# Performance work log

Measured on AMD Instinct MI355X. Metric: run time of the kernel, lower is better.

The kernel has to match this reference:

```python
import jax, jax.numpy as jnp
import numpy as np

SCORE_THRESHOLD = 0.5
GRID = 512  # spatial extent per axis; batch in {0,1} so keys fit int32
SENTINEL = np.int32(2 ** 30)  # larger than any real key (< 2**28)


def _encode(coords):
    # coords: [N,4] int32 (batch, x, y, z) -> unique int32 key
    c = coords.astype(jnp.int32)
    return ((c[:, 0] * GRID + c[:, 1]) * GRID + c[:, 2]) * GRID + c[:, 3]


def _decode_np(k):
    z = k % GRID; k = k // GRID
    y = k % GRID; k = k // GRID
    x = k % GRID; b = k // GRID
    return np.stack([b, x, y, z], axis=1).astype(np.int32)


def setup_inputs() -> dict:
    rng = np.random.default_rng(0)
    Nx, Nm, Dx = 2_000_000, 2_000_000, 16
    # draw unique coordinate keys (MinkowskiEngine coords are unique per tensor)
    keys = np.unique(rng.integers(0, 2 * GRID ** 3, size=3 * Nx, dtype=np.int64)).astype(np.int32)
    rng.shuffle(keys)
    x_keys = keys[:Nx]
    m_keys = np.concatenate([x_keys[: Nm // 2], keys[Nx: Nx + Nm - Nm // 2]])
    rng.shuffle(m_keys)
    key = jax.random.key(0)
    k1, k2 = jax.random.split(key)
    return {
        "x_C": jnp.asarray(_decode_np(x_keys)),
        "x_F": jax.random.normal(k1, (Nx, Dx), dtype=jnp.float32),
        "m_C": jnp.asarray(_decode_np(m_keys)),
        "m_F": jax.random.uniform(k2, (Nm, 1), dtype=jnp.float32),
    }


def _gather_on_union(keys, feats, union_keys):
    # scatter each tensor's features onto the union coordinate set (zeros elsewhere)
    n = keys.shape[0]
    order = jnp.argsort(keys)
    ks = keys[order]
    fs = feats[order]
    pos = jnp.searchsorted(ks, union_keys)
    pc = jnp.clip(pos, 0, n - 1)
    found = (pos < n) & (ks[pc] == union_keys)
    return jnp.where(found[:, None], fs[pc], jnp.zeros((), feats.dtype))


def reference(x_C, x_F, m_C, m_F):
    Nx, Nm = x_F.shape[0], m_F.shape[0]
    xk = _encode(x_C)
    mk = _encode(m_C)
    # coordinate union (ME sparse-tensor addition); fixed size Nx+Nm, padded w/ sentinel
    uk = jnp.unique(jnp.concatenate([xk, mk]), size=Nx + Nm, fill_value=SENTINEL)
    xf = _gather_on_union(xk, x_F, uk)   # x features on union coords  [Nu, Dx]
    mf = _gather_on_union(mk, m_F, uk)   # mask scores on union coords [Nu, 1]
    # target = score above threshold AND x has any positive feature at this coord
    target = (mf[:, 0] > SCORE_THRESHOLD) & (xf > 0).any(axis=1)
    # prune expressed as fixed-shape masking (padding rows have target=False)
    return xf * target[:, None].astype(xf.dtype)
```

## Files before the change

kernel.cpp:

```cpp
#include <hip/hip_runtime.h>
#include <stdint.h>

#define KEYSPACE     (1u << 28)
#define NBUCKET      2048u
#define BUCKET_KEYS  (KEYSPACE / NBUCKET)
#define BUCKET_WORDS (BUCKET_KEYS / 16u)
#define BUCKET_CAP   4096u
#define EPB          8192
#define UMASK        0x55555555u
#define RECS_CAP     1024u

__device__ __forceinline__ uint32_t encode4(int4 c) {
    return ((((uint32_t)c.x * 512u + (uint32_t)c.y) * 512u + (uint32_t)c.z) * 512u) + (uint32_t)c.w;
}
__device__ __forceinline__ uint32_t swz(uint32_t w) { return w ^ ((w >> 5) & 31u); }

__global__ __launch_bounds__(256) void bin_zero(const int* __restrict__ xC,
                                                const int* __restrict__ mC,
                                                const float* __restrict__ mF,
                                                uint2* __restrict__ barr,
                                                uint32_t* __restrict__ bcnt,
                                                float* __restrict__ out,
                                                uint32_t out4, int Nx, int Nm) {
    __shared__ uint32_t hist[NBUCKET];
    __shared__ uint32_t base_[NBUCKET];
    int t = threadIdx.x;
    int blk = blockIdx.x;
    uint32_t nthr = gridDim.x * 256u;

    {
        uint4 z = make_uint4(0u, 0u, 0u, 0u);
        uint4* o4 = reinterpret_cast<uint4*>(out);
        for (uint32_t q = (uint32_t)blk * 256u + t; q < out4; q += nthr) o4[q] = z;
    }

    int total = Nx + Nm;
    int start = blk * EPB;
    int end = min(start + EPB, total);

    for (int q = t; q < (int)NBUCKET; q += 256) hist[q] = 0u;
    __syncthreads();

    for (int e = start + t; e < end; e += 256) {
        uint32_t k = (e < Nx) ? encode4(reinterpret_cast<const int4*>(xC)[e])
                              : encode4(reinterpret_cast<const int4*>(mC)[e - Nx]);
        atomicAdd(&hist[k >> 17], 1u);
    }
    __syncthreads();

    for (int q = t; q < (int)NBUCKET; q += 256) {
        uint32_t h = hist[q];
        base_[q] = h ? atomicAdd(&bcnt[q], h) : 0u;
        hist[q] = 0u;
    }
    __syncthreads();

    for (int e = start + t; e < end; e += 256) {
        uint32_t k; uint2 pl;
        if (e < Nx) {
            k = encode4(reinterpret_cast<const int4*>(xC)[e]);
            pl.x = (k & (BUCKET_KEYS - 1u)) | (1u << 18);
            pl.y = (uint32_t)e;
        } else {
            int j = e - Nx;
            k = encode4(reinterpret_cast<const int4*>(mC)[j]);
            pl.x = (k & (BUCKET_KEYS - 1u)) | ((mF[j] > 0.5f) ? (1u << 17) : 0u);
            pl.y = 0u;
        }
        uint32_t b = k >> 17;
        uint32_t pos = base_[b] + atomicAdd(&hist[b], 1u);
        barr[(size_t)b * BUCKET_CAP + pos] = pl;
    }
}

__global__ __launch_bounds__(256) void build_bucket(const uint2* __restrict__ barr,
                                                    const uint32_t* __restrict__ bcnt,
                                                    uint2* __restrict__ records,
                                                    uint32_t* __restrict__ rcount,
                                                    uint32_t* __restrict__ Btot) {
    __shared__ uint32_t bmp[BUCKET_WORDS];
    __shared__ uint32_t gpre[512];
    __shared__ uint32_t sdata[256];
    __shared__ uint2 recs[RECS_CAP];
    __shared__ uint32_t nrec, rbase;
    int t = threadIdx.x;
    uint32_t b = blockIdx.x;

    {
        uint4 z = make_uint4(0u, 0u, 0u, 0u);
        uint4* bz = reinterpret_cast<uint4*>(bmp);
        for (int q = t; q < (int)(BUCKET_WORDS / 4u); q += 256) bz[q] = z;
    }
    __syncthreads();

    uint32_t n = bcnt[b];
    const uint2* ba = barr + (size_t)b * BUCKET_CAP;

    for (uint32_t e = t; e < n; e += 256u) {
        uint32_t pl = ba[e].x;
        uint32_t off = pl & (BUCKET_KEYS - 1u);
        uint32_t bits = 1u | (((pl >> 17) & 1u) << 1);
        atomicOr(&bmp[swz(off >> 4)], bits << ((off & 15u) * 2u));
    }
    __syncthreads();

    uint32_t c0 = 0u, c1 = 0u;
    {
        uint32_t b0 = 32u * (uint32_t)t, b1 = b0 + 16u;
#pragma unroll
        for (uint32_t q = 0; q < 16u; ++q) c0 += __popc(bmp[swz(b0 + q)] & UMASK);
#pragma unroll
        for (uint32_t q = 0; q < 16u; ++q) c1 += __popc(bmp[swz(b1 + q)] & UMASK);
    }
    uint32_t s = c0 + c1;
    sdata[t] = s;
    __syncthreads();
    for (int off = 1; off < 256; off <<= 1) {
        uint32_t tmp = (t >= off) ? sdata[t - off] : 0u;
        __syncthreads();
        sdata[t] += tmp;
        __syncthreads();
    }
    uint32_t ex = sdata[t] - s;
    gpre[2 * t] = ex;
    gpre[2 * t + 1] = ex + c0;
    if (t == 255) Btot[b] = sdata[255];
    if (t == 0) nrec = 0u;
    __syncthreads();

    for (uint32_t e = t; e < n; e += 256u) {
        uint2 pe = ba[e];
        if (!(pe.x & (1u << 18))) continue;
        uint32_t off = pe.x & (BUCKET_KEYS - 1u);
        uint32_t w = off >> 4;
        uint32_t j2 = (off & 15u) * 2u;
        uint32_t word = bmp[swz(w)];
        if (!((word >> (j2 + 1u)) & 1u)) continue;
        uint32_t g = off >> 8;
        uint32_t r = gpre[g];
        for (uint32_t q = g << 4; q < w; ++q) r += __popc(bmp[swz(q)] & UMASK);
        r += __popc(word & UMASK & ((1u << j2) - 1u));
        uint32_t pos = atomicAdd(&nrec, 1u);
        if (pos < RECS_CAP) recs[pos] = make_uint2(pe.y, (b << 17) | r);
    }
    __syncthreads();

    if (t == 0) rbase = atomicAdd(rcount, min(nrec, RECS_CAP));
    __syncthreads();
    uint32_t n2 = min(nrec, RECS_CAP);
    for (uint32_t q = t; q < n2; q += 256u) records[rbase + q] = recs[q];
}

__global__ __launch_bounds__(1024) void scan_top(const uint32_t* __restrict__ Btot,
                                                 uint32_t* __restrict__ Boff) {
    __shared__ uint32_t sdata[1024];
    int t = threadIdx.x;
    uint32_t v0 = Btot[2 * t], v1 = Btot[2 * t + 1];
    uint32_t s = v0 + v1;
    sdata[t] = s;
    __syncthreads();
    for (int off = 1; off < 1024; off <<= 1) {
        uint32_t tmp = (t >= off) ? sdata[t - off] : 0u;
        __syncthreads();
        sdata[t] += tmp;
        __syncthreads();
    }
    uint32_t ex = sdata[t] - s;
    Boff[2 * t] = ex;
    Boff[2 * t + 1] = ex + v0;
}

__global__ __launch_bounds__(256) void gather_rows(const uint2* __restrict__ records,
                                                   const uint32_t* __restrict__ rcount,
                                                   const uint32_t* __restrict__ Boff,
                                                   const float* __restrict__ xF,
                                                   float* __restrict__ out) {
    uint32_t i = blockIdx.x * blockDim.x + threadIdx.x;
    if (i >= *rcount) return;
    uint2 rec = records[i];
    uint32_t r = Boff[rec.y >> 17] + (rec.y & (BUCKET_KEYS - 1u));

    const float4* f = reinterpret_cast<const float4*>(xF + (size_t)rec.x * 16u);
    float4 f0 = f[0], f1 = f[1], f2 = f[2], f3 = f[3];
    bool any =
        (f0.x > 0.f) | (f0.y > 0.f) | (f0.z > 0.f) | (f0.w > 0.f) |
        (f1.x > 0.f) | (f1.y > 0.f) | (f1.z > 0.f) | (f1.w > 0.f) |
        (f2.x > 0.f) | (f2.y > 0.f) | (f2.z > 0.f) | (f2.w > 0.f) |
        (f3.x > 0.f) | (f3.y > 0.f) | (f3.z > 0.f) | (f3.w > 0.f);
    if (!any) return;

    float4* o = reinterpret_cast<float4*>(out + (size_t)r * 16u);
    o[0] = f0; o[1] = f1; o[2] = f2; o[3] = f3;
}

extern "C" void kernel_launch(void* const* d_in, const int* in_sizes, int n_in,
                              void* d_out, int out_size, void* d_ws, size_t ws_size,
                              hipStream_t stream) {
    const int* xC = (const int*)d_in[0];
    const float* xF = (const float*)d_in[1];
    const int* mC = (const int*)d_in[2];
    const float* mF = (const float*)d_in[3];
    float* out = (float*)d_out;

    int Nx = in_sizes[1] / 16;
    int Nm = in_sizes[3];
    int total = Nx + Nm;
    uint32_t out4 = (uint32_t)(out_size / 4);

    uint8_t* ws = (uint8_t*)d_ws;
    uint2*    barr    = (uint2*)(ws);
    uint2*    records = (uint2*)(ws + (size_t)64 * 1024 * 1024);
    uint32_t* bcnt    = (uint32_t*)(ws + (size_t)80 * 1024 * 1024);
    uint32_t* rcount  = (uint32_t*)(ws + (size_t)80 * 1024 * 1024 + 8192);
    uint32_t* Btot    = (uint32_t*)(ws + (size_t)80 * 1024 * 1024 + 12288);
    uint32_t* Boff    = (uint32_t*)(ws + (size_t)80 * 1024 * 1024 + 20480);

    hipMemsetAsync(bcnt, 0, 8192 + 4, stream);

    int nbin = (total + EPB - 1) / EPB;
    bin_zero<<<nbin, 256, 0, stream>>>(xC, mC, mF, barr, bcnt, out, out4, Nx, Nm);
    build_bucket<<<NBUCKET, 256, 0, stream>>>(barr, bcnt, records, rcount, Btot);
    scan_top<<<1, 1024, 0, stream>>>(Btot, Boff);
    gather_rows<<<(Nx + 255) / 256, 256, 0, stream>>>(records, rcount, Boff, xF, out);
}
```

Baseline: 522.8 us.

## Replace block-local histogram binning with global atomics and use wave-aggregated record output

The binning kernel drops its two-pass shared-memory histogram and now does one pass in a grid-stride loop, taking each slot with a direct global atomicAdd on the bucket counter. This removes the second coordinate read and the block synchronisations, but every element now hits the same 2048 global counters, which risks contention. build_bucket drops its shared record staging buffer and its capacity cap, writing records directly with one wave-level ballot plus one atomic per wave. gather_rows becomes a grid-stride loop over a fixed grid.

Result: slower. 1.502 ms (+187.3%).

```diff
diff --git a/kernel.cpp b/kernel.cpp
--- a/kernel.cpp
+++ b/kernel.cpp
@@ -6,9 +6,7 @@
 #define BUCKET_KEYS  (KEYSPACE / NBUCKET)
 #define BUCKET_WORDS (BUCKET_KEYS / 16u)
 #define BUCKET_CAP   4096u
-#define EPB          8192
 #define UMASK        0x55555555u
-#define RECS_CAP     1024u
 
 __device__ __forceinline__ uint32_t encode4(int4 c) {
     return ((((uint32_t)c.x * 512u + (uint32_t)c.y) * 512u + (uint32_t)c.z) * 512u) + (uint32_t)c.w;
@@ -22,40 +20,17 @@
                                                 uint32_t* __restrict__ bcnt,
                                                 float* __restrict__ out,
                                                 uint32_t out4, int Nx, int Nm) {
-    __shared__ uint32_t hist[NBUCKET];
-    __shared__ uint32_t base_[NBUCKET];
-    int t = threadIdx.x;
-    int blk = blockIdx.x;
+    uint32_t gtid = blockIdx.x * 256u + threadIdx.x;
     uint32_t nthr = gridDim.x * 256u;
 
     {
         uint4 z = make_uint4(0u, 0u, 0u, 0u);
         uint4* o4 = reinterpret_cast<uint4*>(out);
-        for (uint32_t q = (uint32_t)blk * 256u + t; q < out4; q += nthr) o4[q] = z;
+        for (uint32_t q = gtid; q < out4; q += nthr) o4[q] = z;
     }
 
     int total = Nx + Nm;
-    int start = blk * EPB;
-    int end = min(start + EPB, total);
-
-    for (int q = t; q < (int)NBUCKET; q += 256) hist[q] = 0u;
-    __syncthreads();
-
-    for (int e = start + t; e < end; e += 256) {
-        uint32_t k = (e < Nx) ? encode4(reinterpret_cast<const int4*>(xC)[e])
-                              : encode4(reinterpret_cast<const int4*>(mC)[e - Nx]);
-        atomicAdd(&hist[k >> 17], 1u);
-    }
-    __syncthreads();
-
-    for (int q = t; q < (int)NBUCKET; q += 256) {
-        uint32_t h = hist[q];
-        base_[q] = h ? atomicAdd(&bcnt[q], h) : 0u;
-        hist[q] = 0u;
-    }
-    __syncthreads();
-
-    for (int e = start + t; e < end; e += 256) {
+    for (int e = (int)gtid; e < total; e += (int)nthr) {
         uint32_t k; uint2 pl;
         if (e < Nx) {
             k = encode4(reinterpret_cast<const int4*>(xC)[e]);
@@ -68,7 +43,7 @@
             pl.y = 0u;
         }
         uint32_t b = k >> 17;
-        uint32_t pos = base_[b] + atomicAdd(&hist[b], 1u);
+        uint32_t pos = atomicAdd(&bcnt[b], 1u);
         barr[(size_t)b * BUCKET_CAP + pos] = pl;
     }
 }
@@ -81,9 +56,8 @@
     __shared__ uint32_t bmp[BUCKET_WORDS];
     __shared__ uint32_t gpre[512];
     __shared__ uint32_t sdata[256];
-    __shared__ uint2 recs[RECS_CAP];
-    __shared__ uint32_t nrec, rbase;
     int t = threadIdx.x;
+    uint32_t lane = (uint32_t)(t & 63);
     uint32_t b = blockIdx.x;
 
     {
@@ -125,30 +99,42 @@
     gpre[2 * t] = ex;
     gpre[2 * t + 1] = ex + c0;
     if (t == 255) Btot[b] = sdata[255];
-    if (t == 0) nrec = 0u;
-    __syncthreads();
-
-    for (uint32_t e = t; e < n; e += 256u) {
-        uint2 pe = ba[e];
-        if (!(pe.x & (1u << 18))) continue;
-        uint32_t off = pe.x & (BUCKET_KEYS - 1u);
-        uint32_t w = off >> 4;
-        uint32_t j2 = (off & 15u) * 2u;
-        uint32_t word = bmp[swz(w)];
-        if (!((word >> (j2 + 1u)) & 1u)) continue;
-        uint32_t g = off >> 8;
-        uint32_t r = gpre[g];
-        for (uint32_t q = g << 4; q < w; ++q) r += __popc(bmp[swz(q)] & UMASK);
-        r += __popc(word & UMASK & ((1u << j2) - 1u));
-        uint32_t pos = atomicAdd(&nrec, 1u);
-        if (pos < RECS_CAP) recs[pos] = make_uint2(pe.y, (b << 17) | r);
-    }
-    __syncthreads();
-
-    if (t == 0) rbase = atomicAdd(rcount, min(nrec, RECS_CAP));
-    __syncthreads();
-    uint32_t n2 = min(nrec, RECS_CAP);
-    for (uint32_t q = t; q < n2; q += 256u) records[rbase + q] = recs[q];
+    __syncthreads();
+
+    uint32_t nAlign = (n + 255u) & ~255u;
+    for (uint32_t e = t; e < nAlign; e += 256u) {
+        bool survive = false;
+        uint32_t row = 0u, rk = 0u;
+        if (e < n) {
+            uint2 pe = ba[e];
+            if (pe.x & (1u << 18)) {
+                uint32_t off = pe.x & (BUCKET_KEYS - 1u);
+                uint32_t w = off >> 4;
+                uint32_t j2 = (off & 15u) * 2u;
+                uint32_t word = bmp[swz(w)];
+                if ((word >> (j2 + 1u)) & 1u) {
+                    uint32_t g = off >> 8;
+                    uint32_t r = gpre[g];
+                    for (uint32_t q = g << 4; q < w; ++q) r += __popc(bmp[swz(q)] & UMASK);
+                    r += __popc(word & UMASK & ((1u << j2) - 1u));
+                    survive = true;
+                    row = pe.y;
+                    rk = (b << 17) | r;
+                }
+            }
+        }
+        unsigned long long mask = __ballot(survive);
+        uint32_t cnt = (uint32_t)__popcll(mask);
+        if (cnt) {
+            uint32_t base = 0u;
+            if (lane == 0) base = atomicAdd(rcount, cnt);
+            base = (uint32_t)__shfl((int)base, 0, 64);
+            if (survive) {
+                uint32_t mypos = base + (uint32_t)__popcll(mask & ((1ull << lane) - 1ull));
+                records[mypos] = make_uint2(row, rk);
+            }
+        }
+    }
 }
 
 __global__ __launch_bounds__(1024) void scan_top(const uint32_t* __restrict__ Btot,
@@ -175,22 +161,22 @@
                                                    const uint32_t* __restrict__ Boff,
                                                    const float* __restrict__ xF,
                                                    float* __restrict__ out) {
-    uint32_t i = blockIdx.x * blockDim.x + threadIdx.x;
-    if (i >= *rcount) return;
-    uint2 rec = records[i];
-    uint32_t r = Boff[rec.y >> 17] + (rec.y & (BUCKET_KEYS - 1u));
-
-    const float4* f = reinterpret_cast<const float4*>(xF + (size_t)rec.x * 16u);
-    float4 f0 = f[0], f1 = f[1], f2 = f[2], f3 = f[3];
-    bool any =
-        (f0.x > 0.f) | (f0.y > 0.f) | (f0.z > 0.f) | (f0.w > 0.f) |
-        (f1.x > 0.f) | (f1.y > 0.f) | (f1.z > 0.f) | (f1.w > 0.f) |
-        (f2.x > 0.f) | (f2.y > 0.f) | (f2.z > 0.f) | (f2.w > 0.f) |
-        (f3.x > 0.f) | (f3.y > 0.f) | (f3.z > 0.f) | (f3.w > 0.f);
-    if (!any) return;
-
-    float4* o = reinterpret_cast<float4*>(out + (size_t)r * 16u);
-    o[0] = f0; o[1] = f1; o[2] = f2; o[3] = f3;
+    uint32_t nr = *rcount;
+    uint32_t nthr = gridDim.x * 256u;
+    for (uint32_t i = blockIdx.x * 256u + threadIdx.x; i < nr; i += nthr) {
+        uint2 rec = records[i];
+        uint32_t r = Boff[rec.y >> 17] + (rec.y & (BUCKET_KEYS - 1u));
+        const float4* f = reinterpret_cast<const float4*>(xF + (size_t)rec.x * 16u);
+        float4 f0 = f[0], f1 = f[1], f2 = f[2], f3 = f[3];
+        bool any =
+            (f0.x > 0.f) | (f0.y > 0.f) | (f0.z > 0.f) | (f0.w > 0.f) |
+            (f1.x > 0.f) | (f1.y > 0.f) | (f1.z > 0.f) | (f1.w > 0.f) |
+            (f2.x > 0.f) | (f2.y > 0.f) | (f2.z > 0.f) | (f2.w > 0.f) |
+            (f3.x > 0.f) | (f3.y > 0.f) | (f3.z > 0.f) | (f3.w > 0.f);
+        if (!any) continue;
+        float4* o = reinterpret_cast<float4*>(out + (size_t)r * 16u);
+        o[0] = f0; o[1] = f1; o[2] = f2; o[3] = f3;
+    }
 }
 
 extern "C" void kernel_launch(void* const* d_in, const int* in_sizes, int n_in,
@@ -204,7 +190,6 @@
 
     int Nx = in_sizes[1] / 16;
     int Nm = in_sizes[3];
-    int total = Nx + Nm;
     uint32_t out4 = (uint32_t)(out_size / 4);
 
     uint8_t* ws = (uint8_t*)d_ws;
@@ -217,9 +202,8 @@
 
     hipMemsetAsync(bcnt, 0, 8192 + 4, stream);
 
-    int nbin = (total + EPB - 1) / EPB;
-    bin_zero<<<nbin, 256, 0, stream>>>(xC, mC, mF, barr, bcnt, out, out4, Nx, Nm);
+    bin_zero<<<2048, 256, 0, stream>>>(xC, mC, mF, barr, bcnt, out, out4, Nx, Nm);
     build_bucket<<<NBUCKET, 256, 0, stream>>>(barr, bcnt, records, rcount, Btot);
     scan_top<<<1, 1024, 0, stream>>>(Btot, Boff);
-    gather_rows<<<(Nx + 255) / 256, 256, 0, stream>>>(records, rcount, Boff, xF, out);
-}
+    gather_rows<<<2048, 256, 0, stream>>>(records, rcount, Boff, xF, out);
+}
```
